# Kernel optimization log

Measured on AMD Instinct MI355X. Metric: run time of the kernel, lower is better.

Reference implementation:

```python
import jax, jax.numpy as jnp
import numpy as np

N = 100000   # nodes
E = 500000   # edges per relation
R = 3        # relations (etypes)
L = 2        # layers
F = 300      # input features
H = 256      # hidden
C = 23       # classes


def setup_inputs() -> dict:
    key = jax.random.key(0)
    ks = jax.random.split(key, 12)
    s = 0.05
    return {
        "x": jax.random.normal(ks[0], (N, F), jnp.float32),
        "edge_src": jax.random.randint(ks[1], (R, E), 0, N, dtype=jnp.int32),
        "edge_dst": jax.random.randint(ks[2], (R, E), 0, N, dtype=jnp.int32),
        "W_feat": jax.random.normal(ks[3], (F, H), jnp.float32) * s,
        "b_feat": jnp.zeros((H,), jnp.float32),
        "g_feat": jnp.ones((H,), jnp.float32),
        "beta_feat": jnp.zeros((H,), jnp.float32),
        "gcn_W": jax.random.normal(ks[4], (L, R, H, H), jnp.float32) * s,
        "gcn_b": jnp.zeros((L, R, H), jnp.float32),
        "skip_W": jax.random.normal(ks[5], (L, H, H), jnp.float32) * s,
        "skip_b": jnp.zeros((L, H), jnp.float32),
        "bn_g": jnp.ones((L, H), jnp.float32),
        "bn_b": jnp.zeros((L, H), jnp.float32),
        "W_c1": jax.random.normal(ks[6], (H, H), jnp.float32) * s,
        "b_c1": jnp.zeros((H,), jnp.float32),
        "g_c": jnp.ones((H,), jnp.float32),
        "beta_c": jnp.zeros((H,), jnp.float32),
        "W_c2": jax.random.normal(ks[7], (H, C), jnp.float32) * s,
        "b_c2": jnp.zeros((C,), jnp.float32),
    }


def _bn(h, g, b):
    # BatchNorm1d, training-mode batch stats (biased var), eps=1e-5
    m = h.mean(0)
    v = jnp.mean((h - m) ** 2, 0)
    return g * (h - m) * jax.lax.rsqrt(v + 1e-5) + b


def _het_forward(x, edge_src, edge_dst, W_feat, b_feat, g_feat, beta_feat,
                 gcn_W, gcn_b, skip_W, skip_b, bn_g, bn_b,
                 W_c1, b_c1, g_c, beta_c, W_c2, b_c2):
    seg = jax.ops.segment_sum
    ones = jnp.ones((E,), jnp.float32)
    # feat_reduce: Linear + BN + ReLU
    h = jax.nn.relu(_bn(x @ W_feat + b_feat, g_feat, beta_feat))  # [N, H]
    for l in range(L):
        h_res = h @ skip_W[l] + skip_b[l]
        rel = []
        for r in range(R):  # per-relation GraphConv (DGL norm='both')
            src, dst = edge_src[r], edge_dst[r]
            dout = jnp.clip(seg(ones, src, num_segments=N), 1.0, None)
            din = jnp.clip(seg(ones, dst, num_segments=N), 1.0, None)
            xs = h * jax.lax.rsqrt(dout)[:, None]          # src-normalize
            m = seg(xs[src], dst, num_segments=N)          # gather-scatter
            m = m * jax.lax.rsqrt(din)[:, None]            # dst-normalize
            rel.append(m @ gcn_W[l, r] + gcn_b[l, r])
        h = jnp.mean(jnp.stack(rel, 0), 0)  # het_combine='mean'
        h = h + h_res
        h = jax.nn.leaky_relu(_bn(h, bn_g[l], bn_b[l]), 0.01)
        # dropout is identity in eval mode
    # classification head
    h = jax.nn.relu(_bn(h @ W_c1 + b_c1, g_c, beta_c))
    return h @ W_c2 + b_c2  # [N, C]


def reference(x, edge_src, edge_dst, W_feat, b_feat, g_feat, beta_feat,
              gcn_W, gcn_b, skip_W, skip_b, bn_g, bn_b,
              W_c1, b_c1, g_c, beta_c, W_c2, b_c2):
    return _het_forward(x, edge_src, edge_dst, W_feat, b_feat, g_feat,
                        beta_feat, gcn_W, gcn_b, skip_W, skip_b, bn_g, bn_b,
                        W_c1, b_c1, g_c, beta_c, W_c2, b_c2)
```

## Files before the change

kernel.cpp:

```cpp
#include <hip/hip_runtime.h>

#define NN 100000
#define EE 500000
#define RR 3
#define LL 2
#define FF 300
#define HH 256
#define CC 23
#define MPAD 100096
#define SCHUNK 2048
#define SNB ((NN + SCHUNK - 1) / SCHUNK)

static inline int cdiv_h(int a, int b) { return (a + b - 1) / b; }

typedef __attribute__((ext_vector_type(8))) short bf16x8;
typedef __attribute__((ext_vector_type(4))) float f32x4;

__device__ inline unsigned short f2bf(float f) {
    union { float f; unsigned int u; } v; v.f = f;
    unsigned int r = v.u + 0x7fff + ((v.u >> 16) & 1);
    return (unsigned short)(r >> 16);
}
__device__ inline float bf2f(unsigned short u) {
    union { unsigned int u; float f; } v; v.u = ((unsigned int)u) << 16;
    return v.f;
}
__device__ inline void gl_lds16(const void* g, void* l) {
    __builtin_amdgcn_global_load_lds((const __attribute__((address_space(1))) unsigned int*)g,
                                     (__attribute__((address_space(3))) unsigned int*)l,
                                     16, 0, 0);
}

__global__ void hist_kernel(const int* __restrict__ src, const int* __restrict__ dst,
                            int* __restrict__ cnt_out, int* __restrict__ cnt_in,
                            int RE, int Eper) {
    int i = blockIdx.x * blockDim.x + threadIdx.x;
    if (i >= RE) return;
    int r = i / Eper;
    atomicAdd(&cnt_out[r * NN + src[i]], 1);
    atomicAdd(&cnt_in[r * NN + dst[i]], 1);
}

__global__ void rs_kernel(const int* __restrict__ cnt_out, const int* __restrict__ cnt_in,
                          float* __restrict__ rs_out, float* __restrict__ rs_in, int total) {
    int i = blockIdx.x * blockDim.x + threadIdx.x;
    if (i >= total) return;
    rs_out[i] = rsqrtf(fmaxf((float)cnt_out[i], 1.0f));
    rs_in[i]  = rsqrtf(fmaxf((float)cnt_in[i], 1.0f));
}

__global__ __launch_bounds__(256) void scan_a(const int* __restrict__ cnt, int* __restrict__ bsum) {
    int r = blockIdx.y, b = blockIdx.x, t = threadIdx.x;
    const int* c = cnt + (size_t)r * NN;
    int base = b * SCHUNK;
    int s = 0;
    for (int i = t; i < SCHUNK; i += 256) {
        int idx = base + i;
        if (idx < NN) s += c[idx];
    }
#pragma unroll
    for (int o = 1; o < 64; o <<= 1) s += __shfl_xor(s, o);
    __shared__ int sh[4];
    if ((t & 63) == 0) sh[t >> 6] = s;
    __syncthreads();
    if (t == 0) bsum[r * SNB + b] = sh[0] + sh[1] + sh[2] + sh[3];
}

__global__ void scan_b(int* __restrict__ bsum, int* __restrict__ offs) {
    int r = threadIdx.x;
    if (r >= RR) return;
    int* bs = bsum + r * SNB;
    int run = 0;
    for (int i = 0; i < SNB; i++) { int v = bs[i]; bs[i] = run; run += v; }
    offs[(size_t)r * (NN + 1) + NN] = run;
}

__global__ __launch_bounds__(256) void scan_c(const int* __restrict__ cnt, const int* __restrict__ bsum,
                                              int* __restrict__ offs, int* __restrict__ cur) {
    int r = blockIdx.y, b = blockIdx.x, t = threadIdx.x;
    const int* c = cnt + (size_t)r * NN;
    int base = b * SCHUNK + t * 8;
    int v[8]; int s = 0;
#pragma unroll
    for (int j = 0; j < 8; j++) {
        int idx = base + j;
        v[j] = (idx < NN) ? c[idx] : 0;
        s += v[j];
    }
    __shared__ int sh[256];
    sh[t] = s;
    __syncthreads();
    for (int d = 1; d < 256; d <<= 1) {
        int x = (t >= d) ? sh[t - d] : 0;
        __syncthreads();
        sh[t] += x;
        __syncthreads();
    }
    int run = sh[t] - s + bsum[r * SNB + b];
    int* orow = offs + (size_t)r * (NN + 1);
    int* crow = cur + (size_t)r * NN;
#pragma unroll
    for (int j = 0; j < 8; j++) {
        int idx = base + j;
        if (idx < NN) { orow[idx] = run; crow[idx] = run; }
        run += v[j];
    }
}

__global__ void fill_kernel(const int* __restrict__ src, const int* __restrict__ dst,
                            const float* __restrict__ rs_out,
                            int* __restrict__ cur, int2* __restrict__ srcw,
                            int RE, int Eper) {
    int i = blockIdx.x * blockDim.x + threadIdx.x;
    if (i >= RE) return;
    int r = i / Eper;
    int d = dst[i];
    int s = src[i];
    float w = rs_out[r * NN + s];
    int pos = atomicAdd(&cur[r * NN + d], 1);
    srcw[(size_t)r * Eper + pos] = make_int2(s, __float_as_int(w));
}

__global__ void convert_x(const float* __restrict__ x, unsigned short* __restrict__ xpad) {
    int row = blockIdx.x;
    int col = threadIdx.x;
    float v = (row < NN && col < FF) ? x[(size_t)row * FF + col] : 0.f;
    xpad[(size_t)row * 320 + col] = f2bf(v);
}

__global__ void wprep_feat(const float* __restrict__ W, unsigned short* __restrict__ Bt) {
    int n = blockIdx.x;
    int k = threadIdx.x;
    float v = (k < FF) ? W[(size_t)k * HH + n] : 0.f;
    Bt[(size_t)n * 320 + k] = f2bf(v);
}

__global__ void wprep_layer(const float* __restrict__ skipW, const float* __restrict__ gcnW,
                            unsigned short* __restrict__ Bt) {
    int idx = blockIdx.x * blockDim.x + threadIdx.x;
    int n = idx >> 10, k = idx & 1023;
    int seg = k >> 8, k2 = k & 255;
    float v = (seg == 0) ? skipW[(size_t)k2 * HH + n]
                         : gcnW[(size_t)(seg - 1) * HH * HH + (size_t)k2 * HH + n] * (1.0f / 3.0f);
    Bt[(size_t)n * 1024 + k] = f2bf(v);
}

__global__ void bias_layer(const float* __restrict__ skip_b, const float* __restrict__ gcn_b,
                           float* __restrict__ bias) {
    int t = threadIdx.x;
    bias[t] = skip_b[t] + (gcn_b[t] + gcn_b[HH + t] + gcn_b[2 * HH + t]) * (1.0f / 3.0f);
}

__global__ void wprep_c1(const float* __restrict__ W, unsigned short* __restrict__ Bt) {
    int idx = blockIdx.x * blockDim.x + threadIdx.x;
    int n = idx >> 8, k = idx & 255;
    Bt[(size_t)n * HH + k] = f2bf(W[(size_t)k * HH + n]);
}

__global__ void wprep_c2(const float* __restrict__ W, unsigned short* __restrict__ Bt) {
    int n = blockIdx.x;
    int k = threadIdx.x;
    float v = (n < CC) ? W[(size_t)k * CC + n] : 0.f;
    Bt[(size_t)n * HH + k] = f2bf(v);
}

__global__ __launch_bounds__(256) void agg_bf16(unsigned short* __restrict__ hcat,
                                                const int* __restrict__ offs_all,
                                                const int2* __restrict__ srcw_all,
                                                const float* __restrict__ rs_in_all) {
    int r = blockIdx.y;
    const int* offs = offs_all + (size_t)r * (NN + 1);
    const int2* srcw = srcw_all + (size_t)r * EE;
    const float* rs_i = rs_in_all + (size_t)r * NN;
    int wave = threadIdx.x >> 6;
    int lane = threadIdx.x & 63;
    int node = blockIdx.x * 4 + wave;
    if (node >= NN) return;
    int s0 = __builtin_amdgcn_readfirstlane(offs[node]);
    int s1 = __builtin_amdgcn_readfirstlane(offs[node + 1]);
    int cnt = s1 - s0;
    const int2* ew = srcw + s0;
    const unsigned short* hb = hcat + lane * 4;
    float a0 = 0.f, a1 = 0.f, a2 = 0.f, a3 = 0.f;
    int k = 0;
    for (; k + 8 <= cnt; k += 8) {
        int2 e[8];
#pragma unroll
        for (int q = 0; q < 8; q++) e[q] = ew[k + q];
        ushort4 hv[8];
#pragma unroll
        for (int q = 0; q < 8; q++) hv[q] = *(const ushort4*)(hb + (size_t)e[q].x * 1024);
#pragma unroll
        for (int q = 0; q < 8; q++) {
            float u = __int_as_float(e[q].y);
            a0 += u * bf2f(hv[q].x); a1 += u * bf2f(hv[q].y);
            a2 += u * bf2f(hv[q].z); a3 += u * bf2f(hv[q].w);
        }
    }
    if (k + 4 <= cnt) {
        int2 e[4];
#pragma unroll
        for (int q = 0; q < 4; q++) e[q] = ew[k + q];
        ushort4 hv[4];
#pragma unroll
        for (int q = 0; q < 4; q++) hv[q] = *(const ushort4*)(hb + (size_t)e[q].x * 1024);
#pragma unroll
        for (int q = 0; q < 4; q++) {
            float u = __int_as_float(e[q].y);
            a0 += u * bf2f(hv[q].x); a1 += u * bf2f(hv[q].y);
            a2 += u * bf2f(hv[q].z); a3 += u * bf2f(hv[q].w);
        }
        k += 4;
    }
    int rem = cnt - k;
    if (rem > 0) {
        int2 e[3];
#pragma unroll
        for (int q = 0; q < 3; q++) {
            int kk = k + q; if (kk > cnt - 1) kk = cnt - 1;
            e[q] = ew[kk];
        }
        ushort4 hv[3];
#pragma unroll
        for (int q = 0; q < 3; q++) hv[q] = *(const ushort4*)(hb + (size_t)e[q].x * 1024);
        float u0 = __int_as_float(e[0].y);
        float u1 = rem > 1 ? __int_as_float(e[1].y) : 0.f;
        float u2 = rem > 2 ? __int_as_float(e[2].y) : 0.f;
        a0 += u0 * bf2f(hv[0].x) + u1 * bf2f(hv[1].x) + u2 * bf2f(hv[2].x);
        a1 += u0 * bf2f(hv[0].y) + u1 * bf2f(hv[1].y) + u2 * bf2f(hv[2].y);
        a2 += u0 * bf2f(hv[0].z) + u1 * bf2f(hv[1].z) + u2 * bf2f(hv[2].z);
        a3 += u0 * bf2f(hv[0].w) + u1 * bf2f(hv[1].w) + u2 * bf2f(hv[2].w);
    }
    float wi = rs_i[node];
    ushort4 o;
    o.x = f2bf(a0 * wi); o.y = f2bf(a1 * wi);
    o.z = f2bf(a2 * wi); o.w = f2bf(a3 * wi);
    *(ushort4*)(hcat + (size_t)node * 1024 + 256 * (r + 1) + lane * 4) = o;
}

__global__ __launch_bounds__(256) void mfma_gemm(const unsigned short* __restrict__ A, int ldA,
                                                 const unsigned short* __restrict__ Bt,
                                                 const float* __restrict__ bias,
                                                 void* __restrict__ Cv, int ldC,
                                                 int Nstore, int K, int c_bf16,
                                                 float* __restrict__ stats) {
    __shared__ unsigned short ldsA[2][128 * 32];
    __shared__ unsigned short ldsB[2][128 * 32];
    int tid = threadIdx.x;
    int w = tid >> 6, lane = tid & 63;
    int quad = lane >> 4, lr = lane & 15;
    int bm = blockIdx.y * 128, bn = blockIdx.x * 128;
    int wm = w >> 1, wn = w & 1;
    int lrow = lane >> 2;
    int lslot = lane & 3;

    f32x4 acc[4][4];
#pragma unroll
    for (int i = 0; i < 4; i++)
#pragma unroll
        for (int j = 0; j < 4; j++) acc[i][j] = (f32x4){0.f, 0.f, 0.f, 0.f};

    for (int k0 = 0; k0 < K; k0 += 64) {
#pragma unroll
        for (int h = 0; h < 2; h++) {
            int kk0 = k0 + h * 32;
#pragma unroll
            for (int c = 0; c < 2; c++) {
                int cc = w * 2 + c;
                int rA = cc * 16 + lrow;
                int cg = lslot ^ ((rA >> 1) & 3);
                gl_lds16(A + (size_t)(bm + rA) * ldA + kk0 + cg * 8, &ldsA[h][cc * 512]);
                gl_lds16(Bt + (size_t)(bn + rA) * K + kk0 + cg * 8, &ldsB[h][cc * 512]);
            }
        }
        __syncthreads();
#pragma unroll
        for (int h = 0; h < 2; h++) {
            bf16x8 af[4], bfr[4];
#pragma unroll
            for (int i = 0; i < 4; i++) {
                int r = wm * 64 + i * 16 + lr;
                int s = quad ^ ((r >> 1) & 3);
                af[i] = *(const bf16x8*)&ldsA[h][r * 32 + s * 8];
            }
#pragma unroll
            for (int j = 0; j < 4; j++) {
                int n = wn * 64 + j * 16 + lr;
                int s = quad ^ ((n >> 1) & 3);
                bfr[j] = *(const bf16x8*)&ldsB[h][n * 32 + s * 8];
            }
#pragma unroll
            for (int i = 0; i < 4; i++)
#pragma unroll
                for (int j = 0; j < 4; j++)
                    acc[i][j] = __builtin_amdgcn_mfma_f32_16x16x32_bf16(af[i], bfr[j], acc[i][j], 0, 0, 0);
        }
        __syncthreads();
    }

    float* Cf = (float*)Cv;
    unsigned short* Cb = (unsigned short*)Cv;
#pragma unroll
    for (int j = 0; j < 4; j++) {
        int col = bn + wn * 64 + j * 16 + lr;
        if (col >= Nstore) continue;
        float bv = bias ? bias[col] : 0.f;
        float ssum = 0.f, ssq = 0.f;
#pragma unroll
        for (int i = 0; i < 4; i++) {
#pragma unroll
            for (int v = 0; v < 4; v++) {
                int row = bm + wm * 64 + i * 16 + quad * 4 + v;
                if (row < NN) {
                    float val = acc[i][j][v] + bv;
                    if (c_bf16) Cb[(size_t)row * ldC + col] = f2bf(val);
                    else        Cf[(size_t)row * ldC + col] = val;
                    ssum += val; ssq += val * val;
                }
            }
        }
        if (stats) {
            ssum += __shfl_xor(ssum, 16); ssum += __shfl_xor(ssum, 32);
            ssq  += __shfl_xor(ssq, 16);  ssq  += __shfl_xor(ssq, 32);
            if (quad == 0) {
                atomicAdd(&stats[col], ssum);
                atomicAdd(&stats[HH + col], ssq);
            }
        }
    }
}

__global__ void bn_coef(const float* __restrict__ stats, const float* __restrict__ g,
                        const float* __restrict__ b, float* __restrict__ coef, float invM) {
    int c = threadIdx.x;
    float mean = stats[c] * invM;
    float var = stats[HH + c] * invM - mean * mean;
    float inv = rsqrtf(var + 1e-5f);
    float sc = g[c] * inv;
    coef[c] = sc;
    coef[HH + c] = b[c] - mean * sc;
}

__global__ __launch_bounds__(256) void bn_apply_v(const unsigned short* __restrict__ Z,
                                                  const float* __restrict__ coef,
                                                  unsigned short* __restrict__ out, int act) {
    int idx = blockIdx.x * blockDim.x + threadIdx.x;
    if (idx >= NN * 32) return;
    int row = idx >> 5, cg = (idx & 31) * 8;
    union { uint4 u; unsigned short s[8]; } zin, zo;
    zin.u = *(const uint4*)(Z + (size_t)row * HH + cg);
    f32x4 sc0 = *(const f32x4*)(coef + cg);
    f32x4 sc1 = *(const f32x4*)(coef + cg + 4);
    f32x4 sh0 = *(const f32x4*)(coef + HH + cg);
    f32x4 sh1 = *(const f32x4*)(coef + HH + cg + 4);
#pragma unroll
    for (int j = 0; j < 8; j++) {
        float sc = (j < 4) ? sc0[j] : sc1[j - 4];
        float sh = (j < 4) ? sh0[j] : sh1[j - 4];
        float v = bf2f(zin.s[j]) * sc + sh;
        if (act == 1) v = fmaxf(v, 0.f);
        else v = (v < 0.f) ? 0.01f * v : v;
        zo.s[j] = f2bf(v);
    }
    *(uint4*)(out + (size_t)row * 1024 + cg) = zo.u;
}

extern "C" void kernel_launch(void* const* d_in, const int* in_sizes, int n_in,
                              void* d_out, int out_size, void* d_ws, size_t ws_size,
                              hipStream_t stream) {
    const float* x        = (const float*)d_in[0];
    const int*   esrc     = (const int*)d_in[1];
    const int*   edst     = (const int*)d_in[2];
    const float* W_feat   = (const float*)d_in[3];
    const float* b_feat   = (const float*)d_in[4];
    const float* g_feat   = (const float*)d_in[5];
    const float* beta_feat= (const float*)d_in[6];
    const float* gcn_W    = (const float*)d_in[7];
    const float* gcn_b    = (const float*)d_in[8];
    const float* skip_W   = (const float*)d_in[9];
    const float* skip_b   = (const float*)d_in[10];
    const float* bn_g     = (const float*)d_in[11];
    const float* bn_b     = (const float*)d_in[12];
    const float* W_c1     = (const float*)d_in[13];
    const float* b_c1     = (const float*)d_in[14];
    const float* g_c      = (const float*)d_in[15];
    const float* beta_c   = (const float*)d_in[16];
    const float* W_c2     = (const float*)d_in[17];
    const float* b_c2     = (const float*)d_in[18];
    float* out = (float*)d_out;
    (void)in_sizes; (void)n_in; (void)out_size; (void)ws_size;

    char* w = (char*)d_ws;
    size_t off = 0;
    auto alloc = [&](size_t bytes) { void* p = w + off; off += (bytes + 255) & ~(size_t)255; return p; };
    unsigned short* hcat = (unsigned short*)alloc((size_t)MPAD * 1024 * 2);
    unsigned short* xpad = hcat;
    unsigned short* c_acc = (unsigned short*)alloc((size_t)NN * HH * 2);
    float* f_stats = (float*)alloc(4 * 2 * HH * 4);
    float* f_coef  = (float*)alloc(2 * HH * 4);
    float* f_rs_out = (float*)alloc((size_t)RR * NN * 4);
    float* f_rs_in  = (float*)alloc((size_t)RR * NN * 4);
    int* i_cnt_out = (int*)alloc((size_t)RR * NN * 4);
    int* i_cnt_in  = (int*)alloc((size_t)RR * NN * 4);
    int* i_off     = (int*)alloc((size_t)RR * (NN + 1) * 4);
    int* i_cur     = (int*)alloc((size_t)RR * NN * 4);
    int2* i_srcw   = (int2*)alloc((size_t)RR * EE * 8);
    int* i_bsum    = (int*)alloc((size_t)RR * SNB * 4);
    unsigned short* Bt_feat = (unsigned short*)alloc(256 * 320 * 2);
    unsigned short* Bt_l0   = (unsigned short*)alloc(256 * 1024 * 2);
    unsigned short* Bt_l1   = (unsigned short*)alloc(256 * 1024 * 2);
    unsigned short* Bt_c1   = (unsigned short*)alloc(256 * 256 * 2);
    unsigned short* Bt_c2   = (unsigned short*)alloc(128 * 256 * 2);
    float* bias_l0 = (float*)alloc(HH * 4);
    float* bias_l1 = (float*)alloc(HH * 4);

    const float invM = 1.0f / (float)NN;
    const int RE = RR * EE;

    (void)hipMemsetAsync(i_cnt_out, 0, (size_t)RR * NN * 4, stream);
    (void)hipMemsetAsync(i_cnt_in, 0, (size_t)RR * NN * 4, stream);
    (void)hipMemsetAsync(f_stats, 0, 4 * 2 * HH * 4, stream);
    hist_kernel<<<cdiv_h(RE, 256), 256, 0, stream>>>(esrc, edst, i_cnt_out, i_cnt_in, RE, EE);
    rs_kernel<<<cdiv_h(RR * NN, 256), 256, 0, stream>>>(i_cnt_out, i_cnt_in, f_rs_out, f_rs_in, RR * NN);
    scan_a<<<dim3(SNB, RR), 256, 0, stream>>>(i_cnt_in, i_bsum);
    scan_b<<<1, 64, 0, stream>>>(i_bsum, i_off);
    scan_c<<<dim3(SNB, RR), 256, 0, stream>>>(i_cnt_in, i_bsum, i_off, i_cur);
    fill_kernel<<<cdiv_h(RE, 256), 256, 0, stream>>>(esrc, edst, f_rs_out, i_cur, i_srcw, RE, EE);

    convert_x<<<MPAD, 320, 0, stream>>>(x, xpad);
    wprep_feat<<<256, 320, 0, stream>>>(W_feat, Bt_feat);
    wprep_layer<<<1024, 256, 0, stream>>>(skip_W, gcn_W, Bt_l0);
    wprep_layer<<<1024, 256, 0, stream>>>(skip_W + (size_t)HH * HH, gcn_W + (size_t)RR * HH * HH, Bt_l1);
    bias_layer<<<1, 256, 0, stream>>>(skip_b, gcn_b, bias_l0);
    bias_layer<<<1, 256, 0, stream>>>(skip_b + HH, gcn_b + (size_t)RR * HH, bias_l1);
    wprep_c1<<<256, 256, 0, stream>>>(W_c1, Bt_c1);
    wprep_c2<<<128, 256, 0, stream>>>(W_c2, Bt_c2);

    dim3 grid_H(2, MPAD / 128);
    dim3 grid_C(1, MPAD / 128);
    const int nblk_a = cdiv_h(NN * 32, 256);
    float* st0 = f_stats;
    float* st1 = f_stats + 2 * HH;
    float* st2 = f_stats + 4 * HH;
    float* st3 = f_stats + 6 * HH;

    mfma_gemm<<<grid_H, 256, 0, stream>>>(xpad, 320, Bt_feat, b_feat, c_acc, HH, HH, 320, 1, st0);
    bn_coef<<<1, 256, 0, stream>>>(st0, g_feat, beta_feat, f_coef, invM);
    bn_apply_v<<<nblk_a, 256, 0, stream>>>(c_acc, f_coef, hcat, 1);

    for (int l = 0; l < LL; l++) {
        agg_bf16<<<dim3(cdiv_h(NN, 4), RR), 256, 0, stream>>>(hcat, i_off, i_srcw, f_rs_in);
        float* st = l ? st2 : st1;
        mfma_gemm<<<grid_H, 256, 0, stream>>>(hcat, 1024, l ? Bt_l1 : Bt_l0,
                                              l ? bias_l1 : bias_l0, c_acc, HH, HH, 1024, 1, st);
        bn_coef<<<1, 256, 0, stream>>>(st, bn_g + (size_t)l * HH, bn_b + (size_t)l * HH, f_coef, invM);
        bn_apply_v<<<nblk_a, 256, 0, stream>>>(c_acc, f_coef, hcat, 2);
    }

    mfma_gemm<<<grid_H, 256, 0, stream>>>(hcat, 1024, Bt_c1, b_c1, c_acc, HH, HH, 256, 1, st3);
    bn_coef<<<1, 256, 0, stream>>>(st3, g_c, beta_c, f_coef, invM);
    bn_apply_v<<<nblk_a, 256, 0, stream>>>(c_acc, f_coef, hcat + 256, 1);
    mfma_gemm<<<grid_C, 256, 0, stream>>>(hcat + 256, 1024, Bt_c2, b_c2, out, CC, CC, 256, 0, nullptr);
}
```

Measured before the change: 1.231 ms.

## Restructure MFMA GEMM to 128x256 tiles with triple-buffered async LDS pipeline

The GEMM now uses 512-thread blocks, each covering the full 256-wide output row tile, so the A tile is loaded once instead of twice across two column blocks. K-tiles are staged into LDS through a three-buffer ring, with explicit vmcnt waits so global-to-LDS loads overlap the MFMA work, and s_setprio is raised around the MFMA bursts. The aggregation output now uses nontemporal stores, and the C2 weight prep is padded to 256 columns. The trade-offs are much larger LDS use (about 144KB per block) and fewer blocks resident per CU, plus wasted MFMA work on the 23-class head.

New measurement: 1.343 ms. +9.1%, slower.

```diff
diff --git a/kernel.cpp b/kernel.cpp
--- a/kernel.cpp
+++ b/kernel.cpp
@@ -15,6 +15,7 @@
 
 typedef __attribute__((ext_vector_type(8))) short bf16x8;
 typedef __attribute__((ext_vector_type(4))) float f32x4;
+typedef __attribute__((ext_vector_type(4))) unsigned short u16x4;
 
 __device__ inline unsigned short f2bf(float f) {
     union { float f; unsigned int u; } v; v.f = f;
@@ -232,25 +233,25 @@
         a3 += u0 * bf2f(hv[0].w) + u1 * bf2f(hv[1].w) + u2 * bf2f(hv[2].w);
     }
     float wi = rs_i[node];
-    ushort4 o;
+    u16x4 o;
     o.x = f2bf(a0 * wi); o.y = f2bf(a1 * wi);
     o.z = f2bf(a2 * wi); o.w = f2bf(a3 * wi);
-    *(ushort4*)(hcat + (size_t)node * 1024 + 256 * (r + 1) + lane * 4) = o;
-}
-
-__global__ __launch_bounds__(256) void mfma_gemm(const unsigned short* __restrict__ A, int ldA,
-                                                 const unsigned short* __restrict__ Bt,
-                                                 const float* __restrict__ bias,
-                                                 void* __restrict__ Cv, int ldC,
-                                                 int Nstore, int K, int c_bf16,
-                                                 float* __restrict__ stats) {
-    __shared__ unsigned short ldsA[2][128 * 32];
-    __shared__ unsigned short ldsB[2][128 * 32];
+    __builtin_nontemporal_store(o, (u16x4*)(hcat + (size_t)node * 1024 + 256 * (r + 1) + lane * 4));
+}
+
+__global__ __launch_bounds__(512, 2) void mfma_gemm(const unsigned short* __restrict__ A, int ldA,
+                                                    const unsigned short* __restrict__ Bt,
+                                                    const float* __restrict__ bias,
+                                                    void* __restrict__ Cv, int ldC,
+                                                    int Nstore, int K, int c_bf16,
+                                                    float* __restrict__ stats) {
+    __shared__ unsigned short ldsA[3][128 * 64];
+    __shared__ unsigned short ldsB[3][256 * 64];
     int tid = threadIdx.x;
     int w = tid >> 6, lane = tid & 63;
     int quad = lane >> 4, lr = lane & 15;
-    int bm = blockIdx.y * 128, bn = blockIdx.x * 128;
-    int wm = w >> 1, wn = w & 1;
+    int bm = blockIdx.y * 128;
+    int wm = w >> 2, wn = w & 3;
     int lrow = lane >> 2;
     int lslot = lane & 3;
 
@@ -260,20 +261,40 @@
 #pragma unroll
         for (int j = 0; j < 4; j++) acc[i][j] = (f32x4){0.f, 0.f, 0.f, 0.f};
 
-    for (int k0 = 0; k0 < K; k0 += 64) {
+    const int NT = K >> 6;
+
+    auto stage = [&](int bi, int t) {
+        int k0 = t << 6;
+        int rA = w * 16 + lrow;
+        int cgA = lslot ^ ((rA >> 1) & 3);
 #pragma unroll
         for (int h = 0; h < 2; h++) {
-            int kk0 = k0 + h * 32;
+            gl_lds16(A + (size_t)(bm + rA) * ldA + k0 + h * 32 + cgA * 8,
+                     &ldsA[bi][h * 4096 + w * 512]);
 #pragma unroll
             for (int c = 0; c < 2; c++) {
                 int cc = w * 2 + c;
-                int rA = cc * 16 + lrow;
-                int cg = lslot ^ ((rA >> 1) & 3);
-                gl_lds16(A + (size_t)(bm + rA) * ldA + kk0 + cg * 8, &ldsA[h][cc * 512]);
-                gl_lds16(Bt + (size_t)(bn + rA) * K + kk0 + cg * 8, &ldsB[h][cc * 512]);
+                int rB = cc * 16 + lrow;
+                int cgB = lslot ^ ((rB >> 1) & 3);
+                gl_lds16(Bt + (size_t)rB * K + k0 + h * 32 + cgB * 8,
+                         &ldsB[bi][h * 8192 + cc * 512]);
             }
         }
-        __syncthreads();
+    };
+
+    stage(0, 0);
+    if (NT > 1) stage(1, 1);
+
+    int bi = 0;
+    for (int t = 0; t < NT; t++) {
+        if (t + 1 < NT) asm volatile("s_waitcnt vmcnt(6)" ::: "memory");
+        else            asm volatile("s_waitcnt vmcnt(0)" ::: "memory");
+        __builtin_amdgcn_s_barrier();
+        asm volatile("" ::: "memory");
+        if (t + 2 < NT) {
+            int b2 = bi + 2; if (b2 >= 3) b2 -= 3;
+            stage(b2, t + 2);
+        }
 #pragma unroll
         for (int h = 0; h < 2; h++) {
             bf16x8 af[4], bfr[4];
@@ -281,28 +302,30 @@
             for (int i = 0; i < 4; i++) {
                 int r = wm * 64 + i * 16 + lr;
                 int s = quad ^ ((r >> 1) & 3);
-                af[i] = *(const bf16x8*)&ldsA[h][r * 32 + s * 8];
+                af[i] = *(const bf16x8*)&ldsA[bi][h * 4096 + r * 32 + s * 8];
             }
 #pragma unroll
             for (int j = 0; j < 4; j++) {
                 int n = wn * 64 + j * 16 + lr;
                 int s = quad ^ ((n >> 1) & 3);
-                bfr[j] = *(const bf16x8*)&ldsB[h][n * 32 + s * 8];
+                bfr[j] = *(const bf16x8*)&ldsB[bi][h * 8192 + n * 32 + s * 8];
             }
+            __builtin_amdgcn_s_setprio(1);
 #pragma unroll
             for (int i = 0; i < 4; i++)
 #pragma unroll
                 for (int j = 0; j < 4; j++)
                     acc[i][j] = __builtin_amdgcn_mfma_f32_16x16x32_bf16(af[i], bfr[j], acc[i][j], 0, 0, 0);
-        }
-        __syncthreads();
+            __builtin_amdgcn_s_setprio(0);
+        }
+        bi++; if (bi == 3) bi = 0;
     }
 
     float* Cf = (float*)Cv;
     unsigned short* Cb = (unsigned short*)Cv;
 #pragma unroll
     for (int j = 0; j < 4; j++) {
-        int col = bn + wn * 64 + j * 16 + lr;
+        int col = wn * 64 + j * 16 + lr;
         if (col >= Nstore) continue;
         float bv = bias ? bias[col] : 0.f;
         float ssum = 0.f, ssq = 0.f;
@@ -410,7 +433,7 @@
     unsigned short* Bt_l0   = (unsigned short*)alloc(256 * 1024 * 2);
     unsigned short* Bt_l1   = (unsigned short*)alloc(256 * 1024 * 2);
     unsigned short* Bt_c1   = (unsigned short*)alloc(256 * 256 * 2);
-    unsigned short* Bt_c2   = (unsigned short*)alloc(128 * 256 * 2);
+    unsigned short* Bt_c2   = (unsigned short*)alloc(256 * 256 * 2);
     float* bias_l0 = (float*)alloc(HH * 4);
     float* bias_l1 = (float*)alloc(HH * 4);
 
@@ -434,31 +457,30 @@
     bias_layer<<<1, 256, 0, stream>>>(skip_b, gcn_b, bias_l0);
     bias_layer<<<1, 256, 0, stream>>>(skip_b + HH, gcn_b + (size_t)RR * HH, bias_l1);
     wprep_c1<<<256, 256, 0, stream>>>(W_c1, Bt_c1);
-    wprep_c2<<<128, 256, 0, stream>>>(W_c2, Bt_c2);
-
-    dim3 grid_H(2, MPAD / 128);
-    dim3 grid_C(1, MPAD / 128);
+    wprep_c2<<<256, 256, 0, stream>>>(W_c2, Bt_c2);
+
+    dim3 grid_G(1, MPAD / 128);
     const int nblk_a = cdiv_h(NN * 32, 256);
     float* st0 = f_stats;
     float* st1 = f_stats + 2 * HH;
     float* st2 = f_stats + 4 * HH;
     float* st3 = f_stats + 6 * HH;
 
-    mfma_gemm<<<grid_H, 256, 0, stream>>>(xpad, 320, Bt_feat, b_feat, c_acc, HH, HH, 320, 1, st0);
+    mfma_gemm<<<grid_G, 512, 0, stream>>>(xpad, 320, Bt_feat, b_feat, c_acc, HH, HH, 320, 1, st0);
     bn_coef<<<1, 256, 0, stream>>>(st0, g_feat, beta_feat, f_coef, invM);
     bn_apply_v<<<nblk_a, 256, 0, stream>>>(c_acc, f_coef, hcat, 1);
 
     for (int l = 0; l < LL; l++) {
         agg_bf16<<<dim3(cdiv_h(NN, 4), RR), 256, 0, stream>>>(hcat, i_off, i_srcw, f_rs_in);
         float* st = l ? st2 : st1;
-        mfma_gemm<<<grid_H, 256, 0, stream>>>(hcat, 1024, l ? Bt_l1 : Bt_l0,
+        mfma_gemm<<<grid_G, 512, 0, stream>>>(hcat, 1024, l ? Bt_l1 : Bt_l0,
                                               l ? bias_l1 : bias_l0, c_acc, HH, HH, 1024, 1, st);
         bn_coef<<<1, 256, 0, stream>>>(st, bn_g + (size_t)l * HH, bn_b + (size_t)l * HH, f_coef, invM);
         bn_apply_v<<<nblk_a, 256, 0, stream>>>(c_acc, f_coef, hcat, 2);
     }
 
-    mfma_gemm<<<grid_H, 256, 0, stream>>>(hcat, 1024, Bt_c1, b_c1, c_acc, HH, HH, 256, 1, st3);
+    mfma_gemm<<<grid_G, 512, 0, stream>>>(hcat, 1024, Bt_c1, b_c1, c_acc, HH, HH, 256, 1, st3);
     bn_coef<<<1, 256, 0, stream>>>(st3, g_c, beta_c, f_coef, invM);
     bn_apply_v<<<nblk_a, 256, 0, stream>>>(c_acc, f_coef, hcat + 256, 1);
-    mfma_gemm<<<grid_C, 256, 0, stream>>>(hcat + 256, 1024, Bt_c2, b_c2, out, CC, CC, 256, 0, nullptr);
-}
+    mfma_gemm<<<grid_G, 512, 0, stream>>>(hcat + 256, 1024, Bt_c2, b_c2, out, CC, CC, 256, 0, nullptr);
+}
```
